# Performance work log

Measured on AMD Instinct MI355X. Metric: run time of the kernel, lower is better.

The kernel has to match this reference:

```python
import jax, jax.numpy as jnp
import numpy as np

B, S, D, F, E = 8, 4096, 512, 2048, 8
INIT_LAMBDA = 0.2
LN_EPS = 1e-5
LN_MERGE = 0.03  # scale used when merging layer_norm expert task-vectors


def setup_inputs() -> dict:
    key = jax.random.key(0)
    ks = jax.random.split(key, 12)
    n = lambda k, shp, s=1.0: jax.random.normal(k, shp, dtype=jnp.float32) * s
    return {
        "hidden_states": n(ks[0], (B, S, D)),
        # DictMoEGate (2 hidden layers): fc1 ~ N(0, 0.01), fc2 bias = init_lambda
        "gfc1_w": n(ks[1], (D, D), 0.01),
        "gfc1_b": jnp.zeros((D,), jnp.float32),
        "gfc2_w": n(ks[2], (E, D), 0.01),
        "gfc2_b": jnp.full((E,), INIT_LAMBDA, dtype=jnp.float32),
        # base PositionWiseFeedForward params (torch Linear layout: [out, in])
        "W1": n(ks[3], (F, D), 0.02),
        "b1": jnp.zeros((F,), jnp.float32),
        "W2": n(ks[4], (D, F), 0.02),
        "b2": jnp.zeros((D,), jnp.float32),
        "ln_g": jnp.ones((D,), jnp.float32),
        "ln_b": jnp.zeros((D,), jnp.float32),
        # expert task vectors (expert_sd - base_sd), one per base param
        "tv_W1": n(ks[5], (E, F, D), 0.02),
        "tv_b1": n(ks[6], (E, F), 0.02),
        "tv_W2": n(ks[7], (E, D, F), 0.02),
        "tv_b2": n(ks[8], (E, D), 0.02),
        "tv_ln_g": n(ks[9], (E, D), 0.02),
        "tv_ln_b": n(ks[10], (E, D), 0.02),
    }


def reference(hidden_states, gfc1_w, gfc1_b, gfc2_w, gfc2_b,
              W1, b1, W2, b2, ln_g, ln_b,
              tv_W1, tv_b1, tv_W2, tv_b2, tv_ln_g, tv_ln_b):
    x = hidden_states  # [B, S, D] (batch_first)
    # --- gate: per-token 2-layer MLP, then mean over sequence -> [B, E] ---
    gh = jax.nn.relu(jnp.einsum('bsd,hd->bsh', x, gfc1_w) + gfc1_b)
    g = (jnp.einsum('bsh,eh->bse', gh, gfc2_w) + gfc2_b).mean(axis=1)  # [B, E]
    # --- per-sample merged weights: base + sum_e g[b,e] * task_vector[e] ---
    W1m = W1 + jnp.einsum('be,efd->bfd', g, tv_W1)   # [B, F, D]
    b1m = b1 + g @ tv_b1                              # [B, F]
    W2m = W2 + jnp.einsum('be,edf->bdf', g, tv_W2)   # [B, D, F]
    b2m = b2 + g @ tv_b2                              # [B, D]
    # layer_norm params: sd = param + sum_e (tv_e - param) * 0.03 (gate-independent)
    lng = ln_g + LN_MERGE * (tv_ln_g - ln_g).sum(axis=0)  # [D]
    lnb = ln_b + LN_MERGE * (tv_ln_b - ln_b).sum(axis=0)  # [D]
    # --- PositionWiseFeedForward with per-sample weights (dropout = eval/identity) ---
    h = jax.nn.relu(jnp.einsum('bsd,bfd->bsf', x, W1m) + b1m[:, None, :])  # [B, S, F]
    out = jnp.einsum('bsf,bdf->bsd', h, W2m) + b2m[:, None, :]             # [B, S, D]
    res = x + out
    mu = res.mean(axis=-1, keepdims=True)
    var = res.var(axis=-1, keepdims=True)
    return (res - mu) * jax.lax.rsqrt(var + LN_EPS) * lng + lnb
```

## Files before the change

### kernel.cpp

```cpp
#include <hip/hip_runtime.h>

typedef __bf16 bf16;
typedef __attribute__((ext_vector_type(4))) __bf16 bf16x4;
typedef __attribute__((ext_vector_type(8))) __bf16 bf16x8;
typedef __attribute__((ext_vector_type(4))) float f32x4;

#define LDS16(gp, lp)                                                          \
  __builtin_amdgcn_global_load_lds(                                            \
      (const __attribute__((address_space(1))) void*)(gp),                     \
      (__attribute__((address_space(3))) void*)(lp), 16, 0, 0)

__global__ __launch_bounds__(256) void prep_kernel(const float* __restrict__ x,
                                                   const float* __restrict__ g1w,
                                                   bf16* __restrict__ x_bf,
                                                   bf16* __restrict__ g1w_bf,
                                                   float* __restrict__ ghsum) {
  const int bid = blockIdx.x;
  if (bid < 8320) {
    const float* src = bid < 8192 ? x : g1w;
    bf16* dst = bid < 8192 ? x_bf : g1w_bf;
    const int base = bid < 8192 ? bid : bid - 8192;
    int i = (base * 256 + threadIdx.x) * 8;
    float4 a = *(const float4*)(src + i);
    float4 b = *(const float4*)(src + i + 4);
    bf16x8 v;
    v[0] = (bf16)a.x; v[1] = (bf16)a.y; v[2] = (bf16)a.z; v[3] = (bf16)a.w;
    v[4] = (bf16)b.x; v[5] = (bf16)b.y; v[6] = (bf16)b.z; v[7] = (bf16)b.w;
    *(bf16x8*)(dst + i) = v;
  } else {
    float4 z = make_float4(0.f, 0.f, 0.f, 0.f);
    float* p = ghsum + threadIdx.x * 16;
#pragma unroll
    for (int k = 0; k < 4; ++k) *(float4*)(p + k * 4) = z;
  }
}

template <int MODE, int NT>
__global__ __launch_bounds__(512) void gemm256(const bf16* __restrict__ A,
                                               const bf16* __restrict__ B0, long bstride,
                                               const float* __restrict__ bias, long biasStride,
                                               const float* __restrict__ resid,
                                               float* __restrict__ fout,
                                               bf16* __restrict__ hout) {
  constexpr int K = NT * 32;
  __shared__ __align__(16) bf16 smem[4 * 16384];
  const int tid = threadIdx.x;
  const int lane = tid & 63, wv = tid >> 6;
  const int wm = wv >> 2, wn = wv & 3;
  const int lr = lane & 15, q = lane >> 4;
  const int b = blockIdx.z;
  const long blockM = (long)b * 4096 + (long)blockIdx.x * 256;
  const int blockN = blockIdx.y * 256;
  const bf16* Ab = A + blockM * K;
  const bf16* Bb = B0 + (long)b * bstride + (long)blockN * K;

  const int s4 = lane >> 2;
  const int cch = ((lane & 3) ^ ((s4 >> 1) & 3)) * 8;
  const int gA0 = wv * 2;
  const int qa = q ^ ((lr >> 1) & 3);
  const int aoff = (wm * 128 + lr) * 32 + qa * 8;
  const int boff = (wn * 64 + lr) * 32 + qa * 8;

  f32x4 acc[8][4] = {};

  auto stage = [&](int t) {
    bf16* As = smem + (t & 3) * 16384;
    bf16* Bs = As + 8192;
    const long k0 = (long)t * 32;
#pragma unroll
    for (int li = 0; li < 2; ++li) {
      const int g = gA0 + li;
      LDS16(Ab + (long)(g * 16 + s4) * K + k0 + cch, As + g * 512);
      LDS16(Bb + (long)(g * 16 + s4) * K + k0 + cch, Bs + g * 512);
    }
  };

  stage(0);
  stage(1);
  stage(2);
  asm volatile("s_waitcnt vmcnt(8)" ::: "memory");
  __builtin_amdgcn_s_barrier();
  asm volatile("" ::: "memory");

#pragma unroll 1
  for (int t = 0; t < NT; ++t) {
    if (t + 3 < NT) stage(t + 3);
    const bf16* As = smem + (t & 3) * 16384;
    const bf16* Bs = As + 8192;
    bf16x8 af[8], bfr[4];
#pragma unroll
    for (int j = 0; j < 4; ++j) bfr[j] = *(const bf16x8*)&Bs[boff + j * 512];
#pragma unroll
    for (int i = 0; i < 8; ++i) af[i] = *(const bf16x8*)&As[aoff + i * 512];
#pragma unroll
    for (int i = 0; i < 8; ++i)
#pragma unroll
      for (int j = 0; j < 4; ++j)
        acc[i][j] = __builtin_amdgcn_mfma_f32_16x16x32_bf16(af[i], bfr[j], acc[i][j], 0, 0, 0);
    if (t + 3 < NT)
      asm volatile("s_waitcnt vmcnt(8)" ::: "memory");
    else if (t + 2 < NT)
      asm volatile("s_waitcnt vmcnt(4)" ::: "memory");
    else if (t + 1 < NT)
      asm volatile("s_waitcnt vmcnt(0)" ::: "memory");
    asm volatile("" ::: "memory");
    __builtin_amdgcn_s_barrier();
    asm volatile("" ::: "memory");
  }

  if (MODE == 0) {
#pragma unroll
    for (int j = 0; j < 4; ++j) {
      const int gc = blockN + wn * 64 + j * 16 + lr;
      const float bv = bias[gc];
      float s = 0.f;
#pragma unroll
      for (int i = 0; i < 8; ++i)
#pragma unroll
        for (int r = 0; r < 4; ++r) {
          float v = acc[i][j][r] + bv;
          s += v > 0.f ? v : 0.f;
        }
      s += __shfl_xor(s, 16);
      s += __shfl_xor(s, 32);
      if (q == 0) atomicAdd(&fout[b * 512 + gc], s);
    }
  } else if (MODE == 1) {
    float bvv[4];
#pragma unroll
    for (int j = 0; j < 4; ++j)
      bvv[j] = bias[(long)b * biasStride + blockN + wn * 64 + j * 16 + lr];
#pragma unroll 1
    for (int half = 0; half < 2; ++half) {
      __syncthreads();
      if (wm == half) {
#pragma unroll
        for (int i = 0; i < 8; ++i)
#pragma unroll
          for (int j = 0; j < 4; ++j)
#pragma unroll
            for (int r = 0; r < 4; ++r) {
              const int row = i * 16 + q * 4 + r;
              const int col = wn * 64 + j * 16 + lr;
              float v = acc[i][j][r] + bvv[j];
              smem[row * 256 + col] = (bf16)(v > 0.f ? v : 0.f);
            }
      }
      __syncthreads();
#pragma unroll
      for (int p = 0; p < 8; ++p) {
        const int row = p * 16 + (tid >> 5);
        const int seg = tid & 31;
        *(bf16x8*)&hout[(blockM + half * 128 + row) * 2048 + blockN + seg * 8] =
            *(const bf16x8*)&smem[row * 256 + seg * 8];
      }
    }
  } else {
#pragma unroll
    for (int j = 0; j < 4; ++j) {
      const int gc = blockN + wn * 64 + j * 16 + lr;
      const float bv = bias[(long)b * biasStride + gc];
#pragma unroll
      for (int i = 0; i < 8; ++i)
#pragma unroll
        for (int r = 0; r < 4; ++r) {
          const long gr = blockM + wm * 128 + i * 16 + q * 4 + r;
          fout[gr * 512 + gc] = acc[i][j][r] + bv + resid[gr * 512 + gc];
        }
    }
  }
}

__global__ __launch_bounds__(512) void small_kernel(
    const float* __restrict__ ghsum, const float* __restrict__ g2w,
    const float* __restrict__ g2b, const float* __restrict__ lngI,
    const float* __restrict__ lnbI, const float* __restrict__ tvlg,
    const float* __restrict__ tvlb, const float* __restrict__ b1,
    const float* __restrict__ tvb1, const float* __restrict__ b2,
    const float* __restrict__ tvb2, float* __restrict__ g, float* __restrict__ lng,
    float* __restrict__ lnb, float* __restrict__ b1m, float* __restrict__ b2m) {
  __shared__ float gs[64];
  const int t = threadIdx.x;
  if (t < 64) {
    const int b = t >> 3, e = t & 7;
    float s = 0.f;
    for (int h = 0; h < 512; ++h) s += ghsum[b * 512 + h] * g2w[e * 512 + h];
    float gv = s * (1.f / 4096.f) + g2b[e];
    gs[t] = gv;
    g[t] = gv;
  }
  __syncthreads();
  if (t < 512) {
    float lg = lngI[t], lb = lnbI[t], sg = 0.f, sb = 0.f;
    for (int e = 0; e < 8; ++e) { sg += tvlg[e * 512 + t]; sb += tvlb[e * 512 + t]; }
    lng[t] = lg + 0.03f * (sg - 8.f * lg);
    lnb[t] = lb + 0.03f * (sb - 8.f * lb);
  }
  for (int i = t; i < 8 * 2048; i += 512) {
    const int b = i >> 11, f = i & 2047;
    float s = b1[f];
    for (int e = 0; e < 8; ++e) s += gs[b * 8 + e] * tvb1[e * 2048 + f];
    b1m[i] = s;
  }
  for (int i = t; i < 8 * 512; i += 512) {
    const int b = i >> 9, d = i & 511;
    float s = b2[d];
    for (int e = 0; e < 8; ++e) s += gs[b * 8 + e] * tvb2[e * 512 + d];
    b2m[i] = s;
  }
}

__global__ __launch_bounds__(256) void merge_kernel(
    const float* __restrict__ W1, const float* __restrict__ tvW1,
    const float* __restrict__ W2, const float* __restrict__ tvW2,
    const float* __restrict__ g, bf16* __restrict__ W1m, bf16* __restrict__ W2m) {
  int idx = (blockIdx.x * 256 + threadIdx.x) * 4;
  const float* Wp;
  const float* tvp;
  bf16* outp;
  if (idx < 1048576) {
    Wp = W1; tvp = tvW1; outp = W1m;
  } else {
    idx -= 1048576;
    Wp = W2; tvp = tvW2; outp = W2m;
  }
  float4 w = *(const float4*)(Wp + idx);
  float4 tv[8];
#pragma unroll
  for (int e = 0; e < 8; ++e) tv[e] = *(const float4*)(tvp + (long)e * 1048576 + idx);
#pragma unroll
  for (int b = 0; b < 8; ++b) {
    float4 s = w;
#pragma unroll
    for (int e = 0; e < 8; ++e) {
      const float ge = g[b * 8 + e];
      s.x += ge * tv[e].x; s.y += ge * tv[e].y;
      s.z += ge * tv[e].z; s.w += ge * tv[e].w;
    }
    bf16x4 o;
    o[0] = (bf16)s.x; o[1] = (bf16)s.y; o[2] = (bf16)s.z; o[3] = (bf16)s.w;
    *(bf16x4*)(outp + (long)b * 1048576 + idx) = o;
  }
}

__global__ __launch_bounds__(256) void ln_kernel(float* __restrict__ out,
                                                 const float* __restrict__ lng,
                                                 const float* __restrict__ lnb) {
  const int wv = threadIdx.x >> 6, lane = threadIdx.x & 63;
  const long row = (long)blockIdx.x * 4 + wv;
  float* p = out + row * 512 + lane * 8;
  float4 a = *(float4*)p;
  float4 b = *(float4*)(p + 4);
  float v[8] = {a.x, a.y, a.z, a.w, b.x, b.y, b.z, b.w};
  float s1 = 0.f, s2 = 0.f;
#pragma unroll
  for (int k = 0; k < 8; ++k) { s1 += v[k]; s2 += v[k] * v[k]; }
#pragma unroll
  for (int off = 32; off > 0; off >>= 1) {
    s1 += __shfl_xor(s1, off);
    s2 += __shfl_xor(s2, off);
  }
  const float mean = s1 * (1.f / 512.f);
  const float var = s2 * (1.f / 512.f) - mean * mean;
  const float rstd = rsqrtf(var + 1e-5f);
  const int c = lane * 8;
  float o[8];
#pragma unroll
  for (int k = 0; k < 8; ++k) o[k] = (v[k] - mean) * rstd * lng[c + k] + lnb[c + k];
  *(float4*)p = make_float4(o[0], o[1], o[2], o[3]);
  *(float4*)(p + 4) = make_float4(o[4], o[5], o[6], o[7]);
}

extern "C" void kernel_launch(void* const* d_in, const int* in_sizes, int n_in,
                              void* d_out, int out_size, void* d_ws, size_t ws_size,
                              hipStream_t stream) {
  const float* x    = (const float*)d_in[0];
  const float* g1w  = (const float*)d_in[1];
  const float* g1b  = (const float*)d_in[2];
  const float* g2w  = (const float*)d_in[3];
  const float* g2b  = (const float*)d_in[4];
  const float* W1   = (const float*)d_in[5];
  const float* b1   = (const float*)d_in[6];
  const float* W2   = (const float*)d_in[7];
  const float* b2   = (const float*)d_in[8];
  const float* lngI = (const float*)d_in[9];
  const float* lnbI = (const float*)d_in[10];
  const float* tvW1 = (const float*)d_in[11];
  const float* tvb1 = (const float*)d_in[12];
  const float* tvW2 = (const float*)d_in[13];
  const float* tvb2 = (const float*)d_in[14];
  const float* tvlg = (const float*)d_in[15];
  const float* tvlb = (const float*)d_in[16];
  float* out = (float*)d_out;

  char* w = (char*)d_ws;
  bf16*  x_bf   = (bf16*)(w);
  bf16*  g1w_bf = (bf16*)(w + 33554432);
  bf16*  W1m    = (bf16*)(w + 34078720);
  bf16*  W2m    = (bf16*)(w + 50855936);
  bf16*  h      = (bf16*)(w + 67633152);
  float* ghsum  = (float*)(w + 201850880);
  float* g      = (float*)(w + 201867264);
  float* b1m    = (float*)(w + 201867520);
  float* b2m    = (float*)(w + 201933056);
  float* lng    = (float*)(w + 201949440);
  float* lnb    = (float*)(w + 201951488);

  prep_kernel<<<8321, 256, 0, stream>>>(x, g1w, x_bf, g1w_bf, ghsum);
  gemm256<0, 16><<<dim3(16, 2, 8), 512, 0, stream>>>(x_bf, g1w_bf, 0, g1b, 0,
                                                     nullptr, ghsum, nullptr);
  small_kernel<<<1, 512, 0, stream>>>(ghsum, g2w, g2b, lngI, lnbI, tvlg, tvlb,
                                      b1, tvb1, b2, tvb2, g, lng, lnb, b1m, b2m);
  merge_kernel<<<2048, 256, 0, stream>>>(W1, tvW1, W2, tvW2, g, W1m, W2m);
  gemm256<1, 16><<<dim3(16, 8, 8), 512, 0, stream>>>(x_bf, W1m, 1048576, b1m, 2048,
                                                     nullptr, nullptr, h);
  gemm256<2, 64><<<dim3(16, 2, 8), 512, 0, stream>>>(h, W2m, 1048576, b2m, 512,
                                                     x, out, nullptr);
  ln_kernel<<<8192, 256, 0, stream>>>(out, lng, lnb);
}
```

Baseline: 460.9 us.

## Split GEMM mainloop into two phases with interleaved loads and MFMA priority

The GEMM main loop now issues the A and B prefetches separately, each placed between half-batches of LDS fragment reads and MFMAs. Workgroup barriers and s_setprio raise wave priority around the MFMA blocks, so memory issue and matrix math overlap better across waves. The grid is also flattened to 1D with batch as the fastest-varying index, which changes block scheduling order and L2 reuse of weights and activations. The extra barriers per iteration add synchronisation cost.

```diff
diff --git a/kernel.cpp b/kernel.cpp
--- a/kernel.cpp
+++ b/kernel.cpp
@@ -48,9 +48,13 @@
   const int lane = tid & 63, wv = tid >> 6;
   const int wm = wv >> 2, wn = wv & 3;
   const int lr = lane & 15, q = lane >> 4;
-  const int b = blockIdx.z;
-  const long blockM = (long)b * 4096 + (long)blockIdx.x * 256;
-  const int blockN = blockIdx.y * 256;
+  const int bid = blockIdx.x;
+  const int b = bid & 7;
+  const int r = bid >> 3;
+  const int mb = r & 15;
+  const int nb = r >> 4;
+  const long blockM = (long)b * 4096 + (long)mb * 256;
+  const int blockN = nb * 256;
   const bf16* Ab = A + blockM * K;
   const bf16* Bb = B0 + (long)b * bstride + (long)blockN * K;
 
@@ -63,49 +67,68 @@
 
   f32x4 acc[8][4] = {};
 
-  auto stage = [&](int t) {
+  auto stageA = [&](int t) {
     bf16* As = smem + (t & 3) * 16384;
-    bf16* Bs = As + 8192;
     const long k0 = (long)t * 32;
 #pragma unroll
     for (int li = 0; li < 2; ++li) {
       const int g = gA0 + li;
       LDS16(Ab + (long)(g * 16 + s4) * K + k0 + cch, As + g * 512);
+    }
+  };
+  auto stageB = [&](int t) {
+    bf16* Bs = smem + (t & 3) * 16384 + 8192;
+    const long k0 = (long)t * 32;
+#pragma unroll
+    for (int li = 0; li < 2; ++li) {
+      const int g = gA0 + li;
       LDS16(Bb + (long)(g * 16 + s4) * K + k0 + cch, Bs + g * 512);
     }
   };
 
-  stage(0);
-  stage(1);
-  stage(2);
+  stageA(0); stageB(0);
+  stageA(1); stageB(1);
+  stageA(2); stageB(2);
   asm volatile("s_waitcnt vmcnt(8)" ::: "memory");
   __builtin_amdgcn_s_barrier();
-  asm volatile("" ::: "memory");
 
 #pragma unroll 1
   for (int t = 0; t < NT; ++t) {
-    if (t + 3 < NT) stage(t + 3);
     const bf16* As = smem + (t & 3) * 16384;
     const bf16* Bs = As + 8192;
     bf16x8 af[8], bfr[4];
 #pragma unroll
     for (int j = 0; j < 4; ++j) bfr[j] = *(const bf16x8*)&Bs[boff + j * 512];
 #pragma unroll
-    for (int i = 0; i < 8; ++i) af[i] = *(const bf16x8*)&As[aoff + i * 512];
-#pragma unroll
-    for (int i = 0; i < 8; ++i)
+    for (int i = 0; i < 4; ++i) af[i] = *(const bf16x8*)&As[aoff + i * 512];
+    if (t + 3 < NT) stageA(t + 3);
+    __builtin_amdgcn_s_barrier();
+    __builtin_amdgcn_s_setprio(1);
+#pragma unroll
+    for (int i = 0; i < 4; ++i)
 #pragma unroll
       for (int j = 0; j < 4; ++j)
         acc[i][j] = __builtin_amdgcn_mfma_f32_16x16x32_bf16(af[i], bfr[j], acc[i][j], 0, 0, 0);
+    __builtin_amdgcn_s_setprio(0);
+    __builtin_amdgcn_s_barrier();
+#pragma unroll
+    for (int i = 4; i < 8; ++i) af[i] = *(const bf16x8*)&As[aoff + i * 512];
+    if (t + 3 < NT) stageB(t + 3);
+    __builtin_amdgcn_s_barrier();
+    __builtin_amdgcn_s_setprio(1);
+#pragma unroll
+    for (int i = 4; i < 8; ++i)
+#pragma unroll
+      for (int j = 0; j < 4; ++j)
+        acc[i][j] = __builtin_amdgcn_mfma_f32_16x16x32_bf16(af[i], bfr[j], acc[i][j], 0, 0, 0);
+    __builtin_amdgcn_s_setprio(0);
     if (t + 3 < NT)
       asm volatile("s_waitcnt vmcnt(8)" ::: "memory");
     else if (t + 2 < NT)
       asm volatile("s_waitcnt vmcnt(4)" ::: "memory");
     else if (t + 1 < NT)
       asm volatile("s_waitcnt vmcnt(0)" ::: "memory");
-    asm volatile("" ::: "memory");
     __builtin_amdgcn_s_barrier();
-    asm volatile("" ::: "memory");
   }
 
   if (MODE == 0) {
@@ -117,8 +140,8 @@
 #pragma unroll
       for (int i = 0; i < 8; ++i)
 #pragma unroll
-        for (int r = 0; r < 4; ++r) {
-          float v = acc[i][j][r] + bv;
+        for (int r2 = 0; r2 < 4; ++r2) {
+          float v = acc[i][j][r2] + bv;
           s += v > 0.f ? v : 0.f;
         }
       s += __shfl_xor(s, 16);
@@ -139,10 +162,10 @@
 #pragma unroll
           for (int j = 0; j < 4; ++j)
 #pragma unroll
-            for (int r = 0; r < 4; ++r) {
-              const int row = i * 16 + q * 4 + r;
+            for (int r2 = 0; r2 < 4; ++r2) {
+              const int row = i * 16 + q * 4 + r2;
               const int col = wn * 64 + j * 16 + lr;
-              float v = acc[i][j][r] + bvv[j];
+              float v = acc[i][j][r2] + bvv[j];
               smem[row * 256 + col] = (bf16)(v > 0.f ? v : 0.f);
             }
       }
@@ -163,9 +186,9 @@
 #pragma unroll
       for (int i = 0; i < 8; ++i)
 #pragma unroll
-        for (int r = 0; r < 4; ++r) {
-          const long gr = blockM + wm * 128 + i * 16 + q * 4 + r;
-          fout[gr * 512 + gc] = acc[i][j][r] + bv + resid[gr * 512 + gc];
+        for (int r2 = 0; r2 < 4; ++r2) {
+          const long gr = blockM + wm * 128 + i * 16 + q * 4 + r2;
+          fout[gr * 512 + gc] = acc[i][j][r2] + bv + resid[gr * 512 + gc];
         }
     }
   }
@@ -307,14 +330,14 @@
   float* lnb    = (float*)(w + 201951488);
 
   prep_kernel<<<8321, 256, 0, stream>>>(x, g1w, x_bf, g1w_bf, ghsum);
-  gemm256<0, 16><<<dim3(16, 2, 8), 512, 0, stream>>>(x_bf, g1w_bf, 0, g1b, 0,
-                                                     nullptr, ghsum, nullptr);
+  gemm256<0, 16><<<256, 512, 0, stream>>>(x_bf, g1w_bf, 0, g1b, 0,
+                                          nullptr, ghsum, nullptr);
   small_kernel<<<1, 512, 0, stream>>>(ghsum, g2w, g2b, lngI, lnbI, tvlg, tvlb,
                                       b1, tvb1, b2, tvb2, g, lng, lnb, b1m, b2m);
   merge_kernel<<<2048, 256, 0, stream>>>(W1, tvW1, W2, tvW2, g, W1m, W2m);
-  gemm256<1, 16><<<dim3(16, 8, 8), 512, 0, stream>>>(x_bf, W1m, 1048576, b1m, 2048,
-                                                     nullptr, nullptr, h);
-  gemm256<2, 64><<<dim3(16, 2, 8), 512, 0, stream>>>(h, W2m, 1048576, b2m, 512,
-                                                     x, out, nullptr);
+  gemm256<1, 16><<<1024, 512, 0, stream>>>(x_bf, W1m, 1048576, b1m, 2048,
+                                           nullptr, nullptr, h);
+  gemm256<2, 64><<<256, 512, 0, stream>>>(h, W2m, 1048576, b2m, 512,
+                                          x, out, nullptr);
   ln_kernel<<<8192, 256, 0, stream>>>(out, lng, lnb);
 }
```

Result: no change. 456.4 us (-1.0%).
